# Kernel tuning notes

Hardware: AMD Instinct MI355X
Metric: run time of the kernel (lower is better)

Reference implementation:

```python
import jax, jax.numpy as jnp
import numpy as np

B, T, D, C = 16, 1500, 768, 1024

def setup_inputs() -> dict:
    key = jax.random.key(0)
    k1, k2 = jax.random.split(key)
    embed = jax.random.normal(k1, (B, T, D), dtype=jnp.float32)
    cluster_centers = jax.random.normal(k2, (C, D), dtype=jnp.float32)
    return {"embed": embed, "cluster_centers": cluster_centers}

def reference(embed, cluster_centers):
    # Faithful to: dists = -torch.cdist(embed, centers, p=2); clusters = dists.argmax(-1)
    # Euclidean distance via ||e||^2 - 2 e.c + ||c||^2 (GEMM-friendly form).
    e_sq = jnp.sum(embed * embed, axis=-1, keepdims=True)            # (b, t, 1)
    c_sq = jnp.sum(cluster_centers * cluster_centers, axis=-1)       # (c,)
    cross = jnp.einsum('btd,cd->btc', embed, cluster_centers)        # (b, t, c)
    d2 = jnp.maximum(e_sq - 2.0 * cross + c_sq, 0.0)
    dists = -jnp.sqrt(d2)                                            # negative L2 distance
    clusters = jnp.argmax(dists, axis=-1)                            # (b, t) int
    return clusters
```

## Files before the change

kernel.cpp:

```cpp
#include <hip/hip_runtime.h>
#include <cstdint>
#include <cstddef>

#define MROWS 24000
#define NCOLS 1024
#define KDIM  768
#define MT 188
#define KT 48
#define NT 4

typedef _Float16 f16x8  __attribute__((ext_vector_type(8)));
typedef float    f32x16 __attribute__((ext_vector_type(16)));

typedef __attribute__((address_space(1))) void as1_void;
typedef __attribute__((address_space(3))) void as3_void;

#define A_BYTES   (188ull*48*8192)
#define B_OFF     A_BYTES
#define B_BYTES   (4ull*48*16384)
#define CH_OFF    (A_BYTES + B_BYTES)
#define PART_OFF  (CH_OFF + 4096)
#define WS_NEED   (PART_OFF + 24064ull*4*8)

__global__ void k_tile_A(const float* __restrict__ E, _Float16* __restrict__ Aw) {
  int bid = blockIdx.x;
  int mt = bid / 48, kt = bid % 48;
  int t = threadIdx.x;
  int r = t >> 1, p = t & 1;
  int row = mt * 128 + r;
  __shared__ _Float16 lh[2][128][8];
  __shared__ _Float16 ll[2][128][8];
  float x[8];
  if (row < MROWS) {
    const float4* s4 = (const float4*)(E + (size_t)row * KDIM + kt * 16 + p * 8);
    float4 v0 = s4[0], v1 = s4[1];
    x[0]=v0.x; x[1]=v0.y; x[2]=v0.z; x[3]=v0.w; x[4]=v1.x; x[5]=v1.y; x[6]=v1.z; x[7]=v1.w;
  } else {
#pragma unroll
    for (int e = 0; e < 8; ++e) x[e] = 0.f;
  }
#pragma unroll
  for (int e = 0; e < 8; ++e) {
    _Float16 h = (_Float16)x[e];
    lh[p][r][e] = h;
    ll[p][r][e] = (_Float16)(x[e] - (float)h);
  }
  __syncthreads();
  const uint4* sh = (const uint4*)&lh[0][0][0];
  const uint4* sl = (const uint4*)&ll[0][0][0];
  uint4* dst = (uint4*)(Aw + (size_t)bid * 4096);
  dst[t]       = sh[t];
  dst[256 + t] = sl[t];
}

__global__ void k_tile_B(const float* __restrict__ C, _Float16* __restrict__ Bw) {
  int bid = blockIdx.x;
  int nt = bid / 48, kt = bid % 48;
  int t = threadIdx.x;
  int c = t >> 1, p = t & 1;
  __shared__ _Float16 lh[2][256][8];
  __shared__ _Float16 ll[2][256][8];
  const float4* s4 = (const float4*)(C + (size_t)(nt * 256 + c) * KDIM + kt * 16 + p * 8);
  float4 v0 = s4[0], v1 = s4[1];
  float x[8] = {v0.x, v0.y, v0.z, v0.w, v1.x, v1.y, v1.z, v1.w};
#pragma unroll
  for (int e = 0; e < 8; ++e) {
    _Float16 h = (_Float16)x[e];
    lh[p][c][e] = h;
    ll[p][c][e] = (_Float16)(x[e] - (float)h);
  }
  __syncthreads();
  const uint4* sh = (const uint4*)&lh[0][0][0];
  const uint4* sl = (const uint4*)&ll[0][0][0];
  uint4* dst = (uint4*)(Bw + (size_t)bid * 8192);
  dst[t]       = sh[t];
  dst[512 + t] = sl[t];
}

__global__ void k_chalf(const float* __restrict__ C, float* __restrict__ ch) {
  int c = blockIdx.x, t = threadIdx.x;
  const float* src = C + (size_t)c * KDIM;
  float sq = 0.f;
#pragma unroll
  for (int i = 0; i < 3; ++i) {
    float x = src[t + i * 256];
    sq = fmaf(x, x, sq);
  }
#pragma unroll
  for (int m = 1; m < 64; m <<= 1) sq += __shfl_xor(sq, m, 64);
  __shared__ float part[4];
  if ((t & 63) == 0) part[t >> 6] = sq;
  __syncthreads();
  if (t == 0) ch[c] = 0.5f * ((part[0] + part[1]) + (part[2] + part[3]));
}

#define MFMA16(a, b, c) __builtin_amdgcn_mfma_f32_32x32x16_f16((a), (b), (c), 0, 0, 0)

__global__ __launch_bounds__(512, 4) void k_gemm(
    const _Float16* __restrict__ Aw, const _Float16* __restrict__ Bw,
    const float* __restrict__ ch, uint2* __restrict__ part) {
  __shared__ float red_v[4][128];
  __shared__ int   red_i[4][128];

  const int bid0 = blockIdx.x;
  const int swz = (bid0 & 7) * 94 + (bid0 >> 3);
  const int nt = swz / MT, mt = swz % MT;

  const int tid = threadIdx.x, lane = tid & 63, wid = tid >> 6;
  const int wm = wid >> 2, wn = wid & 3;
  const int lo5 = lane & 31, p = lane >> 5;

  const char* Ab = (const char*)Aw + (size_t)mt * (48 * 8192);
  const char* Bb = (const char*)Bw + (size_t)nt * (48 * 16384);

  const int offA = p * 2048 + (wm * 64 + lo5) * 16;
  const int offB = p * 4096 + (wn * 64 + lo5) * 16;

  f32x16 acc[2][2] = {};

#pragma unroll 1
  for (int kt = 0; kt < KT; ++kt) {
    const char* ga = Ab + kt * 8192;
    const char* gb = Bb + kt * 16384;
    f16x8 ah0 = *(const f16x8*)(ga + offA);
    f16x8 ah1 = *(const f16x8*)(ga + offA + 512);
    f16x8 al0 = *(const f16x8*)(ga + 4096 + offA);
    f16x8 al1 = *(const f16x8*)(ga + 4096 + offA + 512);
    f16x8 bh0 = *(const f16x8*)(gb + offB);
    f16x8 bh1 = *(const f16x8*)(gb + offB + 512);
    f16x8 bl0 = *(const f16x8*)(gb + 8192 + offB);
    f16x8 bl1 = *(const f16x8*)(gb + 8192 + offB + 512);
    acc[0][0] = MFMA16(ah0, bh0, acc[0][0]);
    acc[0][0] = MFMA16(ah0, bl0, acc[0][0]);
    acc[0][0] = MFMA16(al0, bh0, acc[0][0]);
    acc[1][0] = MFMA16(ah1, bh0, acc[1][0]);
    acc[1][0] = MFMA16(ah1, bl0, acc[1][0]);
    acc[1][0] = MFMA16(al1, bh0, acc[1][0]);
    acc[0][1] = MFMA16(ah0, bh1, acc[0][1]);
    acc[0][1] = MFMA16(ah0, bl1, acc[0][1]);
    acc[0][1] = MFMA16(al0, bh1, acc[0][1]);
    acc[1][1] = MFMA16(ah1, bh1, acc[1][1]);
    acc[1][1] = MFMA16(ah1, bl1, acc[1][1]);
    acc[1][1] = MFMA16(al1, bh1, acc[1][1]);
  }

  int c0 = nt * 256 + wn * 64 + lo5;
  int c1 = c0 + 32;
  float ch0 = ch[c0];
  float ch1 = ch[c1];
#pragma unroll
  for (int mi = 0; mi < 2; ++mi)
#pragma unroll
    for (int q = 0; q < 16; ++q) {
      float s0 = acc[mi][0][q] - ch0;
      float s1 = acc[mi][1][q] - ch1;
      float v = s0; int ix = c0;
      if (s1 > v) { v = s1; ix = c1; }
#pragma unroll
      for (int m = 1; m <= 16; m <<= 1) {
        float ov = __shfl_xor(v, m, 64);
        int   oi = __shfl_xor(ix, m, 64);
        if (ov > v || (ov == v && oi < ix)) { v = ov; ix = oi; }
      }
      if (lo5 == 0) {
        int rr = (q & 3) + ((q >> 2) << 3) + (p << 2);
        int rloc = wm * 64 + mi * 32 + rr;
        red_v[wn][rloc] = v;
        red_i[wn][rloc] = ix;
      }
    }
  __syncthreads();
  if (tid < 128) {
    float v = red_v[0][tid];
    int ix = red_i[0][tid];
#pragma unroll
    for (int w = 1; w < 4; ++w) {
      float ov = red_v[w][tid];
      int oi = red_i[w][tid];
      if (ov > v) { v = ov; ix = oi; }
    }
    int rowg = mt * 128 + tid;
    part[rowg * 4 + nt] = uint2{ __float_as_uint(v), (unsigned)ix };
  }
}

__global__ void k_merge(const uint2* __restrict__ part, int* __restrict__ out) {
  int r = blockIdx.x * 256 + threadIdx.x;
  if (r >= MROWS) return;
  uint2 b0 = part[r * 4];
  float bvv = __uint_as_float(b0.x);
  int bii = (int)b0.y;
#pragma unroll
  for (int j = 1; j < 4; ++j) {
    uint2 pj = part[r * 4 + j];
    float v = __uint_as_float(pj.x);
    if (v > bvv) { bvv = v; bii = (int)pj.y; }
  }
  out[r] = bii;
}

__global__ void k_naive(const float* __restrict__ E, const float* __restrict__ C,
                        int* __restrict__ out) {
  int row = blockIdx.x * 4 + (threadIdx.x >> 6);
  int lane = threadIdx.x & 63;
  const float* e = E + (size_t)row * KDIM;
  float bvv = -3.4e38f;
  int bii = 0;
  for (int c = 0; c < NCOLS; ++c) {
    const float* cc = C + (size_t)c * KDIM;
    float dot = 0.f, csq = 0.f;
    for (int d = lane; d < KDIM; d += 64) {
      float cv = cc[d];
      dot = fmaf(e[d], cv, dot);
      csq = fmaf(cv, cv, csq);
    }
#pragma unroll
    for (int m = 1; m < 64; m <<= 1) {
      dot += __shfl_xor(dot, m, 64);
      csq += __shfl_xor(csq, m, 64);
    }
    float s = dot - 0.5f * csq;
    if (s > bvv) { bvv = s; bii = c; }
  }
  if (lane == 0) out[row] = bii;
}

extern "C" void kernel_launch(void* const* d_in, const int* in_sizes, int n_in,
                              void* d_out, int out_size, void* d_ws, size_t ws_size,
                              hipStream_t stream) {
  const float* embed   = (const float*)d_in[0];
  const float* centers = (const float*)d_in[1];
  int* out = (int*)d_out;

  if (ws_size >= WS_NEED) {
    char* w = (char*)d_ws;
    _Float16* Aw = (_Float16*)w;
    _Float16* Bw = (_Float16*)(w + B_OFF);
    float*    ch = (float*)(w + CH_OFF);
    uint2*  partb = (uint2*)(w + PART_OFF);
    k_tile_A<<<188 * 48, 256, 0, stream>>>(embed, Aw);
    k_tile_B<<<4 * 48, 512, 0, stream>>>(centers, Bw);
    k_chalf<<<1024, 256, 0, stream>>>(centers, ch);
    k_gemm<<<752, 512, 0, stream>>>(Aw, Bw, ch, partb);
    k_merge<<<94, 256, 0, stream>>>(partb, out);
  } else {
    k_naive<<<6000, 256, 0, stream>>>(embed, centers, out);
  }
}
```

Baseline: 184.6 us.

## Triple-buffer GEMM operand loads in registers with MFMA priority boosting

The k-loop now keeps three register sets of A/B fragments. Loads for iteration k+3 are issued while the MFMAs for iteration k run, so global-load latency is hidden by software pipelining rather than only by wave occupancy. MFMA blocks are wrapped in s_setprio to favour issuing matrix instructions. The extra registers force the launch bound down from 4 to 2 blocks per CU, which lowers occupancy in exchange for more overlap within each wave.

Result: slower. 398.3 us (+115.7%).

```diff
diff --git a/kernel.cpp b/kernel.cpp
--- a/kernel.cpp
+++ b/kernel.cpp
@@ -96,7 +96,7 @@
 
 #define MFMA16(a, b, c) __builtin_amdgcn_mfma_f32_32x32x16_f16((a), (b), (c), 0, 0, 0)
 
-__global__ __launch_bounds__(512, 4) void k_gemm(
+__global__ __launch_bounds__(512, 2) void k_gemm(
     const _Float16* __restrict__ Aw, const _Float16* __restrict__ Bw,
     const float* __restrict__ ch, uint2* __restrict__ part) {
   __shared__ float red_v[4][128];
@@ -118,31 +118,58 @@
 
   f32x16 acc[2][2] = {};
 
+  f16x8 ah0_0, ah1_0, al0_0, al1_0, bh0_0, bh1_0, bl0_0, bl1_0;
+  f16x8 ah0_1, ah1_1, al0_1, al1_1, bh0_1, bh1_1, bl0_1, bl1_1;
+  f16x8 ah0_2, ah1_2, al0_2, al1_2, bh0_2, bh1_2, bl0_2, bl1_2;
+
+#define LOADSET(S, kt)                                                        \
+  do {                                                                        \
+    const char* ga_ = Ab + (kt) * 8192;                                       \
+    const char* gb_ = Bb + (kt) * 16384;                                      \
+    ah0_##S = *(const f16x8*)(ga_ + offA);                                    \
+    ah1_##S = *(const f16x8*)(ga_ + offA + 512);                              \
+    al0_##S = *(const f16x8*)(ga_ + 4096 + offA);                             \
+    al1_##S = *(const f16x8*)(ga_ + 4096 + offA + 512);                       \
+    bh0_##S = *(const f16x8*)(gb_ + offB);                                    \
+    bh1_##S = *(const f16x8*)(gb_ + offB + 512);                              \
+    bl0_##S = *(const f16x8*)(gb_ + 8192 + offB);                             \
+    bl1_##S = *(const f16x8*)(gb_ + 8192 + offB + 512);                       \
+  } while (0)
+
+#define MFMASET(S)                                                            \
+  do {                                                                        \
+    __builtin_amdgcn_s_setprio(1);                                            \
+    acc[0][0] = MFMA16(ah0_##S, bh0_##S, acc[0][0]);                          \
+    acc[0][0] = MFMA16(ah0_##S, bl0_##S, acc[0][0]);                          \
+    acc[0][0] = MFMA16(al0_##S, bh0_##S, acc[0][0]);                          \
+    acc[1][0] = MFMA16(ah1_##S, bh0_##S, acc[1][0]);                          \
+    acc[1][0] = MFMA16(ah1_##S, bl0_##S, acc[1][0]);                          \
+    acc[1][0] = MFMA16(al1_##S, bh0_##S, acc[1][0]);                          \
+    acc[0][1] = MFMA16(ah0_##S, bh1_##S, acc[0][1]);                          \
+    acc[0][1] = MFMA16(ah0_##S, bl1_##S, acc[0][1]);                          \
+    acc[0][1] = MFMA16(al0_##S, bh1_##S, acc[0][1]);                          \
+    acc[1][1] = MFMA16(ah1_##S, bh1_##S, acc[1][1]);                          \
+    acc[1][1] = MFMA16(ah1_##S, bl1_##S, acc[1][1]);                          \
+    acc[1][1] = MFMA16(al1_##S, bh1_##S, acc[1][1]);                          \
+    __builtin_amdgcn_s_setprio(0);                                            \
+  } while (0)
+
+  LOADSET(0, 0);
+  LOADSET(1, 1);
+  LOADSET(2, 2);
+
 #pragma unroll 1
-  for (int kt = 0; kt < KT; ++kt) {
-    const char* ga = Ab + kt * 8192;
-    const char* gb = Bb + kt * 16384;
-    f16x8 ah0 = *(const f16x8*)(ga + offA);
-    f16x8 ah1 = *(const f16x8*)(ga + offA + 512);
-    f16x8 al0 = *(const f16x8*)(ga + 4096 + offA);
-    f16x8 al1 = *(const f16x8*)(ga + 4096 + offA + 512);
-    f16x8 bh0 = *(const f16x8*)(gb + offB);
-    f16x8 bh1 = *(const f16x8*)(gb + offB + 512);
-    f16x8 bl0 = *(const f16x8*)(gb + 8192 + offB);
-    f16x8 bl1 = *(const f16x8*)(gb + 8192 + offB + 512);
-    acc[0][0] = MFMA16(ah0, bh0, acc[0][0]);
-    acc[0][0] = MFMA16(ah0, bl0, acc[0][0]);
-    acc[0][0] = MFMA16(al0, bh0, acc[0][0]);
-    acc[1][0] = MFMA16(ah1, bh0, acc[1][0]);
-    acc[1][0] = MFMA16(ah1, bl0, acc[1][0]);
-    acc[1][0] = MFMA16(al1, bh0, acc[1][0]);
-    acc[0][1] = MFMA16(ah0, bh1, acc[0][1]);
-    acc[0][1] = MFMA16(ah0, bl1, acc[0][1]);
-    acc[0][1] = MFMA16(al0, bh1, acc[0][1]);
-    acc[1][1] = MFMA16(ah1, bh1, acc[1][1]);
-    acc[1][1] = MFMA16(ah1, bl1, acc[1][1]);
-    acc[1][1] = MFMA16(al1, bh1, acc[1][1]);
-  }
+  for (int j = 0; j < KT - 3; j += 3) {
+    MFMASET(0); LOADSET(0, j + 3);
+    MFMASET(1); LOADSET(1, j + 4);
+    MFMASET(2); LOADSET(2, j + 5);
+  }
+  MFMASET(0);
+  MFMASET(1);
+  MFMASET(2);
+
+#undef LOADSET
+#undef MFMASET
 
   int c0 = nt * 256 + wn * 64 + lo5;
   int c1 = c0 + 32;
```

## Stage GEMM tiles through double-buffered LDS with async global-to-LDS loads and bigger tiles

Applied to the files above, without the earlier changes.

The GEMM kernel now stages A and B k-tiles into a double-buffered 128 KB shared-memory region using global_load_lds, instead of each wave reading fragments straight from global memory. Each block covers 256 rows instead of 128, giving four row sub-tiles per wave and halving the grid. The loop interleaves prefetch issue, barriers and s_setprio around the MFMA groups to overlap memory traffic with matrix math. This costs occupancy (launch bounds drop to 2 and shared memory use is large) and adds many barriers per k-step.

Measured after the change: 218.1 us. +18.1%, slower.

```diff
diff --git a/kernel.cpp b/kernel.cpp
--- a/kernel.cpp
+++ b/kernel.cpp
@@ -6,8 +6,9 @@
 #define NCOLS 1024
 #define KDIM  768
 #define MT 188
+#define MT2 94
 #define KT 48
-#define NT 4
+#define NK 24
 
 typedef _Float16 f16x8  __attribute__((ext_vector_type(8)));
 typedef float    f32x16 __attribute__((ext_vector_type(16)));
@@ -96,52 +97,119 @@
 
 #define MFMA16(a, b, c) __builtin_amdgcn_mfma_f32_32x32x16_f16((a), (b), (c), 0, 0, 0)
 
-__global__ __launch_bounds__(512, 4) void k_gemm(
+__global__ __launch_bounds__(512, 2) void k_gemm(
     const _Float16* __restrict__ Aw, const _Float16* __restrict__ Bw,
     const float* __restrict__ ch, uint2* __restrict__ part) {
-  __shared__ float red_v[4][128];
-  __shared__ int   red_i[4][128];
+  __shared__ __align__(16) char smem[2][65536];
+  __shared__ float red_v[4][256];
+  __shared__ int   red_i[4][256];
 
   const int bid0 = blockIdx.x;
-  const int swz = (bid0 & 7) * 94 + (bid0 >> 3);
-  const int nt = swz / MT, mt = swz % MT;
+  const int swz = (bid0 & 7) * 47 + (bid0 >> 3);
+  const int nt = swz / MT2, mt2 = swz % MT2;
 
   const int tid = threadIdx.x, lane = tid & 63, wid = tid >> 6;
   const int wm = wid >> 2, wn = wid & 3;
   const int lo5 = lane & 31, p = lane >> 5;
 
-  const char* Ab = (const char*)Aw + (size_t)mt * (48 * 8192);
+  const char* Ab = (const char*)Aw + (size_t)(mt2 * 2) * (48 * 8192);
   const char* Bb = (const char*)Bw + (size_t)nt * (48 * 16384);
 
-  const int offA = p * 2048 + (wm * 64 + lo5) * 16;
-  const int offB = p * 4096 + (wn * 64 + lo5) * 16;
-
-  f32x16 acc[2][2] = {};
+  auto stA = [&](char* wb, int k16, int t, int g) {
+    __builtin_amdgcn_global_load_lds(
+        (as1_void*)(Ab + ((size_t)g * 48 + k16) * 8192 + tid * 16),
+        (as3_void*)(wb + (t * 2 + g) * 8192 + tid * 16), 16, 0, 0);
+  };
+  auto stB = [&](char* wb, int k16, int t, int h) {
+    __builtin_amdgcn_global_load_lds(
+        (as1_void*)(Bb + (size_t)k16 * 16384 + h * 8192 + tid * 16),
+        (as3_void*)(wb + 32768 + t * 16384 + h * 8192 + tid * 16), 16, 0, 0);
+  };
+
+  f32x16 acc[4][2] = {};
+
+  const int offAr = p * 2048 + lo5 * 16;
+  const int offBr = 32768 + p * 4096 + (wn * 64 + lo5) * 16;
+
+  stA(smem[0], 0, 0, 0); stA(smem[0], 0, 0, 1); stB(smem[0], 0, 0, 0); stB(smem[0], 0, 0, 1);
+  stA(smem[0], 1, 1, 0); stA(smem[0], 1, 1, 1); stB(smem[0], 1, 1, 0); stB(smem[0], 1, 1, 1);
 
 #pragma unroll 1
-  for (int kt = 0; kt < KT; ++kt) {
-    const char* ga = Ab + kt * 8192;
-    const char* gb = Bb + kt * 16384;
-    f16x8 ah0 = *(const f16x8*)(ga + offA);
-    f16x8 ah1 = *(const f16x8*)(ga + offA + 512);
-    f16x8 al0 = *(const f16x8*)(ga + 4096 + offA);
-    f16x8 al1 = *(const f16x8*)(ga + 4096 + offA + 512);
-    f16x8 bh0 = *(const f16x8*)(gb + offB);
-    f16x8 bh1 = *(const f16x8*)(gb + offB + 512);
-    f16x8 bl0 = *(const f16x8*)(gb + 8192 + offB);
-    f16x8 bl1 = *(const f16x8*)(gb + 8192 + offB + 512);
-    acc[0][0] = MFMA16(ah0, bh0, acc[0][0]);
-    acc[0][0] = MFMA16(ah0, bl0, acc[0][0]);
-    acc[0][0] = MFMA16(al0, bh0, acc[0][0]);
-    acc[1][0] = MFMA16(ah1, bh0, acc[1][0]);
-    acc[1][0] = MFMA16(ah1, bl0, acc[1][0]);
-    acc[1][0] = MFMA16(al1, bh0, acc[1][0]);
-    acc[0][1] = MFMA16(ah0, bh1, acc[0][1]);
-    acc[0][1] = MFMA16(ah0, bl1, acc[0][1]);
-    acc[0][1] = MFMA16(al0, bh1, acc[0][1]);
-    acc[1][1] = MFMA16(ah1, bh1, acc[1][1]);
-    acc[1][1] = MFMA16(ah1, bl1, acc[1][1]);
-    acc[1][1] = MFMA16(al1, bh1, acc[1][1]);
+  for (int j = 0; j < NK; ++j) {
+    const char* rb = smem[j & 1];
+    char* wb = smem[(j + 1) & 1];
+    const bool pre = (j + 1 < NK);
+    const int nk0 = 2 * (j + 1);
+#pragma unroll
+    for (int t = 0; t < 2; ++t) {
+      if (t == 0 || pre) asm volatile("s_waitcnt vmcnt(4)" ::: "memory");
+      else               asm volatile("s_waitcnt vmcnt(0)" ::: "memory");
+      __builtin_amdgcn_s_barrier();
+
+      const char* at = rb + (t * 2 + wm) * 8192;
+      const char* bt = rb + t * 16384;
+      f16x8 ah0, ah1, al0, al1, bh0, bl0, bh1, bl1;
+
+      ah0 = *(const f16x8*)(at + offAr);
+      ah1 = *(const f16x8*)(at + offAr + 512);
+      al0 = *(const f16x8*)(at + 4096 + offAr);
+      al1 = *(const f16x8*)(at + 4096 + offAr + 512);
+      bh0 = *(const f16x8*)(bt + offBr);
+      bl0 = *(const f16x8*)(bt + 8192 + offBr);
+      if (pre) stA(wb, nk0 + t, t, 0);
+      __builtin_amdgcn_s_barrier();
+      __builtin_amdgcn_s_setprio(1);
+      acc[0][0] = MFMA16(ah0, bh0, acc[0][0]);
+      acc[0][0] = MFMA16(ah0, bl0, acc[0][0]);
+      acc[0][0] = MFMA16(al0, bh0, acc[0][0]);
+      acc[1][0] = MFMA16(ah1, bh0, acc[1][0]);
+      acc[1][0] = MFMA16(ah1, bl0, acc[1][0]);
+      acc[1][0] = MFMA16(al1, bh0, acc[1][0]);
+      __builtin_amdgcn_s_setprio(0);
+      __builtin_amdgcn_s_barrier();
+
+      bh1 = *(const f16x8*)(bt + offBr + 512);
+      bl1 = *(const f16x8*)(bt + 8192 + offBr + 512);
+      if (pre) stA(wb, nk0 + t, t, 1);
+      __builtin_amdgcn_s_barrier();
+      __builtin_amdgcn_s_setprio(1);
+      acc[0][1] = MFMA16(ah0, bh1, acc[0][1]);
+      acc[0][1] = MFMA16(ah0, bl1, acc[0][1]);
+      acc[0][1] = MFMA16(al0, bh1, acc[0][1]);
+      acc[1][1] = MFMA16(ah1, bh1, acc[1][1]);
+      acc[1][1] = MFMA16(ah1, bl1, acc[1][1]);
+      acc[1][1] = MFMA16(al1, bh1, acc[1][1]);
+      __builtin_amdgcn_s_setprio(0);
+      __builtin_amdgcn_s_barrier();
+
+      ah0 = *(const f16x8*)(at + offAr + 1024);
+      ah1 = *(const f16x8*)(at + offAr + 1536);
+      al0 = *(const f16x8*)(at + 4096 + offAr + 1024);
+      al1 = *(const f16x8*)(at + 4096 + offAr + 1536);
+      if (pre) stB(wb, nk0 + t, t, 0);
+      __builtin_amdgcn_s_barrier();
+      __builtin_amdgcn_s_setprio(1);
+      acc[2][1] = MFMA16(ah0, bh1, acc[2][1]);
+      acc[2][1] = MFMA16(ah0, bl1, acc[2][1]);
+      acc[2][1] = MFMA16(al0, bh1, acc[2][1]);
+      acc[3][1] = MFMA16(ah1, bh1, acc[3][1]);
+      acc[3][1] = MFMA16(ah1, bl1, acc[3][1]);
+      acc[3][1] = MFMA16(al1, bh1, acc[3][1]);
+      __builtin_amdgcn_s_setprio(0);
+      __builtin_amdgcn_s_barrier();
+
+      if (pre) stB(wb, nk0 + t, t, 1);
+      __builtin_amdgcn_s_barrier();
+      __builtin_amdgcn_s_setprio(1);
+      acc[2][0] = MFMA16(ah0, bh0, acc[2][0]);
+      acc[2][0] = MFMA16(ah0, bl0, acc[2][0]);
+      acc[2][0] = MFMA16(al0, bh0, acc[2][0]);
+      acc[3][0] = MFMA16(ah1, bh0, acc[3][0]);
+      acc[3][0] = MFMA16(ah1, bl0, acc[3][0]);
+      acc[3][0] = MFMA16(al1, bh0, acc[3][0]);
+      __builtin_amdgcn_s_setprio(0);
+      __builtin_amdgcn_s_barrier();
+    }
   }
 
   int c0 = nt * 256 + wn * 64 + lo5;
@@ -149,7 +217,7 @@
   float ch0 = ch[c0];
   float ch1 = ch[c1];
 #pragma unroll
-  for (int mi = 0; mi < 2; ++mi)
+  for (int mi = 0; mi < 4; ++mi)
 #pragma unroll
     for (int q = 0; q < 16; ++q) {
       float s0 = acc[mi][0][q] - ch0;
@@ -164,13 +232,13 @@
       }
       if (lo5 == 0) {
         int rr = (q & 3) + ((q >> 2) << 3) + (p << 2);
-        int rloc = wm * 64 + mi * 32 + rr;
+        int rloc = wm * 128 + mi * 32 + rr;
         red_v[wn][rloc] = v;
         red_i[wn][rloc] = ix;
       }
     }
   __syncthreads();
-  if (tid < 128) {
+  if (tid < 256) {
     float v = red_v[0][tid];
     int ix = red_i[0][tid];
 #pragma unroll
@@ -179,7 +247,7 @@
       int oi = red_i[w][tid];
       if (ov > v) { v = ov; ix = oi; }
     }
-    int rowg = mt * 128 + tid;
+    int rowg = mt2 * 256 + tid;
     part[rowg * 4 + nt] = uint2{ __float_as_uint(v), (unsigned)ix };
   }
 }
@@ -241,7 +309,7 @@
     k_tile_A<<<188 * 48, 256, 0, stream>>>(embed, Aw);
     k_tile_B<<<4 * 48, 512, 0, stream>>>(centers, Bw);
     k_chalf<<<1024, 256, 0, stream>>>(centers, ch);
-    k_gemm<<<752, 512, 0, stream>>>(Aw, Bw, ch, partb);
+    k_gemm<<<376, 512, 0, stream>>>(Aw, Bw, ch, partb);
     k_merge<<<94, 256, 0, stream>>>(partb, out);
   } else {
     k_naive<<<6000, 256, 0, stream>>>(embed, centers, out);
```

## Restructure GEMM to 4 waves with LDS triple-buffered A and prefetched B

Applied to the files above, without the earlier changes.

Halves the GEMM block to 256 threads, each wave now covering all 128 rows and a 64-column slice. The A tile is staged into a three-slot LDS ring with global_load_lds, and the B fragments are prefetched into registers one k-step ahead, all synchronised by explicit vmcnt waits and barriers. MFMAs run at raised priority. The aim is to hide global-load latency behind MFMA work and to share A across waves instead of having each wave reload it from global memory. The cost is more accumulator registers per wave and fewer waves per block.

New measurement: 193.7 us. +4.9%, slower.

```diff
diff --git a/kernel.cpp b/kernel.cpp
--- a/kernel.cpp
+++ b/kernel.cpp
@@ -96,60 +96,112 @@
 
 #define MFMA16(a, b, c) __builtin_amdgcn_mfma_f32_32x32x16_f16((a), (b), (c), 0, 0, 0)
 
-__global__ __launch_bounds__(512, 4) void k_gemm(
+__global__ __launch_bounds__(256, 2) void k_gemm(
     const _Float16* __restrict__ Aw, const _Float16* __restrict__ Bw,
     const float* __restrict__ ch, uint2* __restrict__ part) {
-  __shared__ float red_v[4][128];
-  __shared__ int   red_i[4][128];
+  __shared__ __align__(16) char smem[3][8192];
+  float (&red_v)[4][128] = *reinterpret_cast<float (*)[4][128]>(&smem[0][0]);
+  int   (&red_i)[4][128] = *reinterpret_cast<int   (*)[4][128]>(&smem[0][2048]);
 
   const int bid0 = blockIdx.x;
   const int swz = (bid0 & 7) * 94 + (bid0 >> 3);
   const int nt = swz / MT, mt = swz % MT;
 
-  const int tid = threadIdx.x, lane = tid & 63, wid = tid >> 6;
-  const int wm = wid >> 2, wn = wid & 3;
+  const int tid = threadIdx.x, lane = tid & 63, wn = tid >> 6;
   const int lo5 = lane & 31, p = lane >> 5;
 
   const char* Ab = (const char*)Aw + (size_t)mt * (48 * 8192);
   const char* Bb = (const char*)Bw + (size_t)nt * (48 * 16384);
 
-  const int offA = p * 2048 + (wm * 64 + lo5) * 16;
+  const int offA = p * 2048 + lo5 * 16;
   const int offB = p * 4096 + (wn * 64 + lo5) * 16;
 
-  f32x16 acc[2][2] = {};
+  auto stageA = [&](char* sb, int kt) {
+    const char* ga = Ab + kt * 8192;
+    __builtin_amdgcn_global_load_lds((as1_void*)(ga + tid * 16),
+                                     (as3_void*)(sb + tid * 16), 16, 0, 0);
+    __builtin_amdgcn_global_load_lds((as1_void*)(ga + 4096 + tid * 16),
+                                     (as3_void*)(sb + 4096 + tid * 16), 16, 0, 0);
+  };
+
+  f32x16 acc[4][2] = {};
+
+  f16x8 b0h0, b0h1, b0l0, b0l1;
+  f16x8 b1h0, b1h1, b1l0, b1l1;
+  f16x8 b2h0, b2h1, b2l0, b2l1;
+
+#define LOADB(S, kt)                                                          \
+  do {                                                                        \
+    const char* gb_ = Bb + (size_t)(kt) * 16384;                              \
+    b##S##h0 = *(const f16x8*)(gb_ + offB);                                   \
+    b##S##h1 = *(const f16x8*)(gb_ + offB + 512);                             \
+    b##S##l0 = *(const f16x8*)(gb_ + 8192 + offB);                            \
+    b##S##l1 = *(const f16x8*)(gb_ + 8192 + offB + 512);                      \
+  } while (0)
+
+#define KSTEP(S, SN, rb, wb, j)                                               \
+  do {                                                                        \
+    if ((j) < KT - 1) asm volatile("s_waitcnt vmcnt(2)" ::: "memory");        \
+    else              asm volatile("s_waitcnt vmcnt(0)" ::: "memory");        \
+    __builtin_amdgcn_s_barrier();                                             \
+    f16x8 ah0 = *(const f16x8*)((rb) + offA);                                 \
+    f16x8 ah1 = *(const f16x8*)((rb) + offA + 512);                           \
+    f16x8 ah2 = *(const f16x8*)((rb) + offA + 1024);                          \
+    f16x8 ah3 = *(const f16x8*)((rb) + offA + 1536);                          \
+    f16x8 al0 = *(const f16x8*)((rb) + 4096 + offA);                          \
+    f16x8 al1 = *(const f16x8*)((rb) + 4096 + offA + 512);                    \
+    f16x8 al2 = *(const f16x8*)((rb) + 4096 + offA + 1024);                   \
+    f16x8 al3 = *(const f16x8*)((rb) + 4096 + offA + 1536);                   \
+    if ((j) + 1 < KT) LOADB(SN, (j) + 1);                                     \
+    if ((j) + 2 < KT) stageA((wb), (j) + 2);                                  \
+    __builtin_amdgcn_s_setprio(1);                                            \
+    acc[0][0] = MFMA16(ah0, b##S##h0, acc[0][0]);   \
+    acc[0][0] = MFMA16(ah0, b##S##l0, acc[0][0]);                             \
+    acc[0][0] = MFMA16(al0, b##S##h0, acc[0][0]);                             \
+    acc[0][1] = MFMA16(ah0, b##S##h1, acc[0][1]);                             \
+    acc[0][1] = MFMA16(ah0, b##S##l1, acc[0][1]);                             \
+    acc[0][1] = MFMA16(al0, b##S##h1, acc[0][1]);                             \
+    acc[1][0] = MFMA16(ah1, b##S##h0, acc[1][0]);                             \
+    acc[1][0] = MFMA16(ah1, b##S##l0, acc[1][0]);                             \
+    acc[1][0] = MFMA16(al1, b##S##h0, acc[1][0]);                             \
+    acc[1][1] = MFMA16(ah1, b##S##h1, acc[1][1]);                             \
+    acc[1][1] = MFMA16(ah1, b##S##l1, acc[1][1]);                             \
+    acc[1][1] = MFMA16(al1, b##S##h1, acc[1][1]);                             \
+    acc[2][0] = MFMA16(ah2, b##S##h0, acc[2][0]);                             \
+    acc[2][0] = MFMA16(ah2, b##S##l0, acc[2][0]);                             \
+    acc[2][0] = MFMA16(al2, b##S##h0, acc[2][0]);                             \
+    acc[2][1] = MFMA16(ah2, b##S##h1, acc[2][1]);                             \
+    acc[2][1] = MFMA16(ah2, b##S##l1, acc[2][1]);                             \
+    acc[2][1] = MFMA16(al2, b##S##h1, acc[2][1]);                             \
+    acc[3][0] = MFMA16(ah3, b##S##h0, acc[3][0]);                             \
+    acc[3][0] = MFMA16(ah3, b##S##l0, acc[3][0]);                             \
+    acc[3][0] = MFMA16(al3, b##S##h0, acc[3][0]);                             \
+    acc[3][1] = MFMA16(ah3, b##S##h1, acc[3][1]);                             \
+    acc[3][1] = MFMA16(ah3, b##S##l1, acc[3][1]);                             \
+    acc[3][1] = MFMA16(al3, b##S##h1, acc[3][1]);                             \
+    __builtin_amdgcn_s_setprio(0);                                            \
+  } while (0)
+
+  LOADB(0, 0);
+  stageA(smem[0], 0);
+  stageA(smem[1], 1);
 
 #pragma unroll 1
-  for (int kt = 0; kt < KT; ++kt) {
-    const char* ga = Ab + kt * 8192;
-    const char* gb = Bb + kt * 16384;
-    f16x8 ah0 = *(const f16x8*)(ga + offA);
-    f16x8 ah1 = *(const f16x8*)(ga + offA + 512);
-    f16x8 al0 = *(const f16x8*)(ga + 4096 + offA);
-    f16x8 al1 = *(const f16x8*)(ga + 4096 + offA + 512);
-    f16x8 bh0 = *(const f16x8*)(gb + offB);
-    f16x8 bh1 = *(const f16x8*)(gb + offB + 512);
-    f16x8 bl0 = *(const f16x8*)(gb + 8192 + offB);
-    f16x8 bl1 = *(const f16x8*)(gb + 8192 + offB + 512);
-    acc[0][0] = MFMA16(ah0, bh0, acc[0][0]);
-    acc[0][0] = MFMA16(ah0, bl0, acc[0][0]);
-    acc[0][0] = MFMA16(al0, bh0, acc[0][0]);
-    acc[1][0] = MFMA16(ah1, bh0, acc[1][0]);
-    acc[1][0] = MFMA16(ah1, bl0, acc[1][0]);
-    acc[1][0] = MFMA16(al1, bh0, acc[1][0]);
-    acc[0][1] = MFMA16(ah0, bh1, acc[0][1]);
-    acc[0][1] = MFMA16(ah0, bl1, acc[0][1]);
-    acc[0][1] = MFMA16(al0, bh1, acc[0][1]);
-    acc[1][1] = MFMA16(ah1, bh1, acc[1][1]);
-    acc[1][1] = MFMA16(ah1, bl1, acc[1][1]);
-    acc[1][1] = MFMA16(al1, bh1, acc[1][1]);
-  }
+  for (int jb = 0; jb < KT; jb += 3) {
+    KSTEP(0, 1, smem[0], smem[2], jb);
+    KSTEP(1, 2, smem[1], smem[0], jb + 1);
+    KSTEP(2, 0, smem[2], smem[1], jb + 2);
+  }
+
+#undef KSTEP
+#undef LOADB
 
   int c0 = nt * 256 + wn * 64 + lo5;
   int c1 = c0 + 32;
   float ch0 = ch[c0];
   float ch1 = ch[c1];
 #pragma unroll
-  for (int mi = 0; mi < 2; ++mi)
+  for (int mi = 0; mi < 4; ++mi)
 #pragma unroll
     for (int q = 0; q < 16; ++q) {
       float s0 = acc[mi][0][q] - ch0;
@@ -164,7 +216,7 @@
       }
       if (lo5 == 0) {
         int rr = (q & 3) + ((q >> 2) << 3) + (p << 2);
-        int rloc = wm * 64 + mi * 32 + rr;
+        int rloc = mi * 32 + rr;
         red_v[wn][rloc] = v;
         red_i[wn][rloc] = ix;
       }
@@ -241,7 +293,7 @@
     k_tile_A<<<188 * 48, 256, 0, stream>>>(embed, Aw);
     k_tile_B<<<4 * 48, 512, 0, stream>>>(centers, Bw);
     k_chalf<<<1024, 256, 0, stream>>>(centers, ch);
-    k_gemm<<<752, 512, 0, stream>>>(Aw, Bw, ch, partb);
+    k_gemm<<<752, 256, 0, stream>>>(Aw, Bw, ch, partb);
     k_merge<<<94, 256, 0, stream>>>(partb, out);
   } else {
     k_naive<<<6000, 256, 0, stream>>>(embed, centers, out);
```
